# Kernel optimization log

Measured on AMD Instinct MI355X. Metric: run time of the kernel, lower is better.

Reference implementation:

```python
import jax, jax.numpy as jnp
import numpy as np

B, S, D_X, D_H = 1024, 512, 128, 128
A_VOCAB, A_EMB, T_VOCAB, T_EMB = 100, 32, 4, 16
GRU_IN = D_X + A_EMB + T_EMB + 1  # 177
Y_IN = D_H + D_X + A_EMB + T_EMB  # 304


def _lin_init(key, d_in, d_out):
    k1, k2 = jax.random.split(key)
    lim = 1.0 / np.sqrt(d_in)
    W = jax.random.uniform(k1, (d_out, d_in), minval=-lim, maxval=lim, dtype=jnp.float32)
    b = jax.random.uniform(k2, (d_out,), minval=-lim, maxval=lim, dtype=jnp.float32)
    return W, b


def setup_inputs() -> dict:
    key = jax.random.key(0)
    ks = jax.random.split(key, 16)
    x = jax.random.normal(ks[0], (B, D_X), dtype=jnp.float32)
    a = jax.random.randint(ks[1], (B, S), 0, A_VOCAB)
    t = jax.random.randint(ks[2], (B, S), 0, T_VOCAB)
    y = jax.random.uniform(ks[3], (B, S), dtype=jnp.float32)
    mask = jnp.ones((B, S), dtype=jnp.float32)

    xW, xb = _lin_init(ks[4], D_X, D_X)                 # x_proj
    a_emb = jax.random.normal(ks[5], (A_VOCAB, A_EMB), dtype=jnp.float32)
    t_emb = jax.random.normal(ks[6], (T_VOCAB, T_EMB), dtype=jnp.float32)
    W_ih, b_ih = _lin_init(ks[7], GRU_IN, 3 * D_H)      # GRUCell input weights
    W_hh, b_hh = _lin_init(ks[8], D_H, 3 * D_H)         # GRUCell hidden weights
    h0W, h0b = _lin_init(ks[9], D_X, D_H)               # h0 MLP
    tW1, tb1 = _lin_init(ks[10], D_H, D_H)              # t_head
    tW2, tb2 = _lin_init(ks[11], D_H, T_VOCAB)
    yW1, yb1 = _lin_init(ks[12], Y_IN, D_H)             # y_head
    yW2, yb2 = _lin_init(ks[13], D_H, 1)
    return {
        'x': x, 'a': a, 't': t, 'y': y, 'mask': mask,
        'xW': xW, 'xb': xb, 'a_emb': a_emb, 't_emb': t_emb,
        'W_ih': W_ih, 'b_ih': b_ih, 'W_hh': W_hh, 'b_hh': b_hh,
        'h0W': h0W, 'h0b': h0b,
        'tW1': tW1, 'tb1': tb1, 'tW2': tW2, 'tb2': tb2,
        'yW1': yW1, 'yb1': yb1, 'yW2': yW2, 'yb2': yb2,
    }


def _crn_forward(x, y, mask, xW, xb, a_emb, t_emb, W_ih, b_ih, W_hh, b_hh,
                 h0W, h0b, tW1, tb1, tW2, tb2, yW1, yb1, yW2, yb2, a, t):
    gelu = lambda v: jax.nn.gelu(v, approximate=False)
    x_enc = x @ xW.T + xb                       # [B, D_X]
    h = jnp.tanh(x_enc @ h0W.T + h0b)           # [B, D_H]
    a_e = a_emb[a]                              # [B, S, A_EMB]
    t_e = t_emb[t]                              # [B, S, T_EMB]
    y3 = y[..., None]                           # [B, S, 1]

    # time-major slices for scan
    a_e_t = jnp.swapaxes(a_e, 0, 1)
    t_e_t = jnp.swapaxes(t_e, 0, 1)
    y_t = jnp.swapaxes(y3, 0, 1)
    m_t = jnp.swapaxes(mask, 0, 1)[..., None]   # [S, B, 1]

    def step(h, inp):
        ae, te, yt, m = inp
        # grad_reverse is identity in forward; dropout off (eval)
        t_logits = gelu(h @ tW1.T + tb1) @ tW2.T + tb2          # [B, T_VOCAB]
        y_in = jnp.concatenate([h, x_enc, ae, te], axis=-1)
        y_logits = gelu(y_in @ yW1.T + yb1) @ yW2.T + yb2        # [B, 1]
        upd = jnp.concatenate([x_enc, ae, te, yt], axis=-1)      # [B, GRU_IN]
        gx = upd @ W_ih.T + b_ih
        gh = h @ W_hh.T + b_hh
        r = jax.nn.sigmoid(gx[:, :D_H] + gh[:, :D_H])
        z = jax.nn.sigmoid(gx[:, D_H:2 * D_H] + gh[:, D_H:2 * D_H])
        n = jnp.tanh(gx[:, 2 * D_H:] + r * gh[:, 2 * D_H:])
        h_next = (1.0 - z) * n + z * h
        h_new = m * h_next + (1.0 - m) * h
        return h_new, (y_logits, t_logits, h)

    _, (y_seq, t_seq, h_seq) = jax.lax.scan(step, h, (a_e_t, t_e_t, y_t, m_t))
    # back to batch-major [B, S, ...]
    return (jnp.swapaxes(y_seq, 0, 1), jnp.swapaxes(t_seq, 0, 1), jnp.swapaxes(h_seq, 0, 1))


def reference(x, a, t, y, mask, xW, xb, a_emb, t_emb, W_ih, b_ih, W_hh, b_hh,
              h0W, h0b, tW1, tb1, tW2, tb2, yW1, yb1, yW2, yb2):
    return _crn_forward(x, y, mask, xW, xb, a_emb, t_emb, W_ih, b_ih, W_hh, b_hh,
                        h0W, h0b, tW1, tb1, tW2, tb2, yW1, yb1, yW2, yb2, a, t)
```

## Files before the change

### kernel.cpp

```cpp
#include <hip/hip_runtime.h>
#include <math.h>

#define SLEN 512

typedef _Float16 half8 __attribute__((ext_vector_type(8)));
typedef _Float16 half2v __attribute__((ext_vector_type(2)));
typedef __fp16 fp16x2 __attribute__((ext_vector_type(2)));
typedef float f32x4 __attribute__((ext_vector_type(4)));
typedef unsigned int uint;

union U4H8 { uint4 u; half8 h; };
union UH2 { uint u; half2v v; fp16x2 p; };

static __device__ __forceinline__ uint packh2(float a, float b){
  UH2 x; x.p = __builtin_amdgcn_cvt_pkrtz(a, b); return x.u;
}
static __device__ __forceinline__ float loh(uint u){ UH2 x; x.u=u; return (float)x.v[0]; }
static __device__ __forceinline__ float hih(uint u){ UH2 x; x.u=u; return (float)x.v[1]; }
static __device__ __forceinline__ half8 ld_h8(const uint* p){
  U4H8 x; x.u = *(const uint4*)p; return x.h;
}
static __device__ __forceinline__ float rcpf(float x){ return __builtin_amdgcn_rcpf(x); }
static __device__ __forceinline__ float sigm(float v){ return rcpf(1.0f+__expf(-v)); }
static __device__ __forceinline__ float tanh_f(float v){ return 1.0f - 2.0f*rcpf(__expf(2.0f*v)+1.0f); }
static __device__ __forceinline__ float gelu_exact(float v){
  return 0.5f*v*(1.0f+erff(v*0.7071067811865475f));
}
#define MFMA(a,b,c) __builtin_amdgcn_mfma_f32_16x16x32_f16((a),(b),(c),0,0,0)

__global__ void k_sample(const float* __restrict__ x, const float* __restrict__ xW, const float* __restrict__ xb,
                         const float* __restrict__ h0W, const float* __restrict__ h0b,
                         const float* __restrict__ W_ih, const float* __restrict__ b_ih, const float* __restrict__ b_hh,
                         const float* __restrict__ yW1, const float* __restrict__ yb1,
                         float* __restrict__ w_h0, float* __restrict__ w_xgx, float* __restrict__ w_yx)
{
  const int b = blockIdx.x, tid = threadIdx.x;
  __shared__ float sx[128];
  __shared__ float sxe[128];
  if (tid < 128) sx[tid] = x[b*128+tid];
  __syncthreads();
  if (tid < 128) {
    float acc = xb[tid];
    #pragma unroll 8
    for (int j=0;j<128;++j) acc += xW[tid*128+j]*sx[j];
    sxe[tid] = acc;
  }
  __syncthreads();
  {
    const int o = tid;
    float acc = b_ih[o] + (o < 256 ? b_hh[o] : 0.f);
    #pragma unroll 8
    for (int j=0;j<128;++j) acc += W_ih[o*177+j]*sxe[j];
    w_xgx[b*384+o] = acc;
  }
  if (tid < 128) {
    float acc = h0b[tid];
    #pragma unroll 8
    for (int j=0;j<128;++j) acc += h0W[tid*128+j]*sxe[j];
    w_h0[b*128+tid] = tanhf(acc);
    float a2 = yb1[tid];
    #pragma unroll 8
    for (int j=0;j<128;++j) a2 += yW1[tid*304+128+j]*sxe[j];
    w_yx[b*128+tid] = a2;
  }
}

__global__ __launch_bounds__(384,1) void k_recur(
  const float* __restrict__ W_hh, const float* __restrict__ W_ih, const float* __restrict__ b_hh,
  const int* __restrict__ a, const int* __restrict__ tt,
  const float* __restrict__ yy, const float* __restrict__ mask,
  const float* __restrict__ w_h0, const float* __restrict__ w_xgx,
  const float* __restrict__ a_emb, const float* __restrict__ t_emb,
  float* __restrict__ o_h, uint* __restrict__ h16)
{
  const int tid = threadIdx.x;
  const int wv = tid>>6, lane = tid&63, q = lane>>4, c = lane&15;
  const int g = wv>>1, H = wv&1;
  const int b0 = blockIdx.x*16;
  const int rowbase = g*128 + H*64;

  __shared__ __align__(16) uint s_h[2][16*68];
  __shared__ __align__(16) uint s_ext[2][16*36];
  __shared__ __align__(16) uint s_rz[2][1024];
  __shared__ __align__(16) uint s_chunk[2][1024];
  __shared__ __align__(16) uint s_al[1600];
  __shared__ __align__(16) uint s_te[32];

  half8 wf[24];
  #pragma unroll
  for (int t4=0;t4<4;++t4) {
    const int row = rowbase + t4*16 + c;
    #pragma unroll
    for (int kt=0;kt<4;++kt) {
      const float4* wp = (const float4*)(W_hh + row*128 + kt*32 + q*8);
      float4 v0 = wp[0], v1 = wp[1];
      half8 hv;
      hv[0]=(_Float16)v0.x; hv[1]=(_Float16)v0.y; hv[2]=(_Float16)v0.z; hv[3]=(_Float16)v0.w;
      hv[4]=(_Float16)v1.x; hv[5]=(_Float16)v1.y; hv[6]=(_Float16)v1.z; hv[7]=(_Float16)v1.w;
      wf[t4*6+kt] = hv;
    }
    #pragma unroll
    for (int kt=4;kt<6;++kt) {
      half8 hv;
      #pragma unroll
      for (int j=0;j<8;++j) {
        int k2 = (kt-4)*32 + q*8 + j;
        float v = (k2 < 49) ? W_ih[row*177 + 128 + k2] : 0.f;
        hv[j] = (_Float16)v;
      }
      wf[t4*6+kt] = hv;
    }
  }
  f32x4 xg[4];
  #pragma unroll
  for (int t4=0;t4<4;++t4)
    #pragma unroll
    for (int r=0;r<4;++r)
      xg[t4][r] = w_xgx[(b0+c)*384 + rowbase + t4*16 + q*4 + r];
  f32x4 bhh[4]; float hm[16];
  if (g==2) {
    #pragma unroll
    for (int t4=0;t4<4;++t4)
      #pragma unroll
      for (int r=0;r<4;++r) {
        bhh[t4][r] = b_hh[256 + H*64 + t4*16 + q*4 + r];
        hm[t4*4+r] = w_h0[(b0+c)*128 + H*64 + t4*16 + q*4 + r];
      }
  }
  for (int d = tid; d < 1600; d += 384) {
    int row = d>>4, col = d&15;
    s_al[d] = packh2(a_emb[row*32+2*col], a_emb[row*32+2*col+1]);
  }
  if (tid < 32) {
    int row = tid>>3, col = tid&7;
    s_te[tid] = packh2(t_emb[row*16+2*col], t_emb[row*16+2*col+1]);
  }
  uint4 cr0, cr1, cr2, cr3;
  if (wv==0) {
    const uint* bp = (q==0) ? (const uint*)a : (q==1) ? (const uint*)tt
                   : (q==2) ? (const uint*)yy : (const uint*)mask;
    const uint4* p = (const uint4*)(bp + (size_t)(b0+c)*512);
    cr0=p[0]; cr1=p[1]; cr2=p[2]; cr3=p[3];
    uint4* dst = (uint4*)&s_chunk[0][q*256 + c*16];
    dst[0]=cr0; dst[1]=cr1; dst[2]=cr2; dst[3]=cr3;
  }
  if (g==2) {
    #pragma unroll
    for (int t4=0;t4<4;++t4) {
      int base = c*68 + H*32 + t4*8 + q*2;
      s_h[0][base]   = packh2(hm[t4*4+0], hm[t4*4+1]);
      s_h[0][base+1] = packh2(hm[t4*4+2], hm[t4*4+3]);
    }
  }
  __syncthreads();
  if (g==0) {
    int av = (int)s_chunk[0][c*16];
    int tv = (int)s_chunk[0][256 + c*16];
    uint yu = s_chunk[0][512 + c*16];
    float yv = __uint_as_float(yu);
    #pragma unroll
    for (int i=0;i<4;++i) {
      int d = H*16 + q*4 + i;
      uint u;
      if (d < 16) u = s_al[av*16 + d];
      else if (d < 24) u = s_te[tv*8 + (d-16)];
      else if (d == 24) u = packh2(yv, 0.f);
      else u = 0u;
      s_ext[0][c*36 + d] = u;
    }
  }
  __syncthreads();

  f32x4 acc[4], acc2[4];

  for (int s=0; s<SLEN; ++s) {
    const int pb = s&1;
    half8 hb[4], eb[2];
    #pragma unroll
    for (int kt=0;kt<4;++kt) hb[kt] = ld_h8(&s_h[pb][c*68 + kt*16 + q*4]);
    #pragma unroll
    for (int e=0;e<2;++e)    eb[e]  = ld_h8(&s_ext[pb][c*36 + e*16 + q*4]);

    if (g < 2) {
      if (g==1 && s>0) {
        const int ob = (s-1)&1;
        const int smp = H*8 + (lane>>3), ch = lane&7;
        const uint* hp = &s_h[ob][smp*68 + ch*8];
        const size_t pr = (size_t)(b0+smp)*SLEN + (s-1);
        if (h16) {
          uint4* hq = (uint4*)(h16 + pr*64 + ch*8);
          hq[0] = *(const uint4*)(hp);
          hq[1] = *(const uint4*)(hp + 4);
        } else {
          float* op = o_h + pr*128 + ch*16;
          #pragma unroll
          for (int i2=0;i2<2;++i2) {
            uint4 u = *(const uint4*)(hp + i2*4);
            float4 f0 = make_float4(loh(u.x), hih(u.x), loh(u.y), hih(u.y));
            float4 f1 = make_float4(loh(u.z), hih(u.z), loh(u.w), hih(u.w));
            *(float4*)(op + i2*8)     = f0;
            *(float4*)(op + i2*8 + 4) = f1;
          }
        }
      }
      #pragma unroll
      for (int t4=0;t4<4;++t4) acc[t4] = xg[t4];
      #pragma unroll
      for (int kt=0;kt<6;++kt) {
        half8 bsel = (kt<4) ? hb[kt] : eb[kt-4];
        #pragma unroll
        for (int t4=0;t4<4;++t4) acc[t4] = MFMA(wf[t4*6+kt], bsel, acc[t4]);
      }
      #pragma unroll
      for (int t4=0;t4<4;++t4)
        #pragma unroll
        for (int pr=0;pr<2;++pr) {
          float s0 = sigm(acc[t4][2*pr]), s1 = sigm(acc[t4][2*pr+1]);
          s_rz[g][(((H*4+t4)*2+pr)*4+q)*16 + c] = packh2(s0, s1);
        }
      if (wv==0) {
        if ((s&15)==8 && s<490) {
          const int s0n = ((s>>4)+1)*16;
          const uint* bp = (q==0) ? (const uint*)a : (q==1) ? (const uint*)tt
                         : (q==2) ? (const uint*)yy : (const uint*)mask;
          const uint4* p = (const uint4*)(bp + (size_t)(b0+c)*512 + s0n);
          cr0=p[0]; cr1=p[1]; cr2=p[2]; cr3=p[3];
        }
        if ((s&15)==9 && s<491) {
          uint4* dst = (uint4*)&s_chunk[((s>>4)+1)&1][q*256 + c*16];
          dst[0]=cr0; dst[1]=cr1; dst[2]=cr2; dst[3]=cr3;
        }
      }
    } else {
      #pragma unroll
      for (int t4=0;t4<4;++t4) { acc[t4] = bhh[t4]; acc2[t4] = xg[t4]; }
      #pragma unroll
      for (int kt=0;kt<4;++kt)
        #pragma unroll
        for (int t4=0;t4<4;++t4) acc[t4] = MFMA(wf[t4*6+kt], hb[kt], acc[t4]);
      #pragma unroll
      for (int kt=4;kt<6;++kt)
        #pragma unroll
        for (int t4=0;t4<4;++t4) acc2[t4] = MFMA(wf[t4*6+kt], eb[kt-4], acc2[t4]);
    }
    __syncthreads();
    if (g==2) {
      const float mval = __uint_as_float(s_chunk[(s>>4)&1][768 + c*16 + (s&15)]);
      #pragma unroll
      for (int t4=0;t4<4;++t4)
        #pragma unroll
        for (int pr=0;pr<2;++pr) {
          const int slot = (((H*4+t4)*2+pr)*4+q)*16 + c;
          uint ru = s_rz[0][slot], zu = s_rz[1][slot];
          const int i0 = t4*4 + 2*pr;
          float n0 = tanh_f(acc2[t4][2*pr]   + loh(ru)*acc[t4][2*pr]);
          float n1 = tanh_f(acc2[t4][2*pr+1] + hih(ru)*acc[t4][2*pr+1]);
          float h0o = hm[i0], h1o = hm[i0+1];
          float hn0 = n0 + loh(zu)*(h0o - n0);
          float hn1 = n1 + hih(zu)*(h1o - n1);
          hm[i0]   = h0o + mval*(hn0 - h0o);
          hm[i0+1] = h1o + mval*(hn1 - h1o);
        }
      const int nb = (s+1)&1;
      #pragma unroll
      for (int t4=0;t4<4;++t4) {
        int base = c*68 + H*32 + t4*8 + q*2;
        s_h[nb][base]   = packh2(hm[t4*4+0], hm[t4*4+1]);
        s_h[nb][base+1] = packh2(hm[t4*4+2], hm[t4*4+3]);
      }
    } else if (g==0 && s < SLEN-1) {
      const int sn = s+1;
      const int par2 = (sn>>4)&1, st = sn&15;
      int av = (int)s_chunk[par2][c*16 + st];
      int tv = (int)s_chunk[par2][256 + c*16 + st];
      float yv = __uint_as_float(s_chunk[par2][512 + c*16 + st]);
      #pragma unroll
      for (int i=0;i<4;++i) {
        int d = H*16 + q*4 + i;
        uint u;
        if (d < 16) u = s_al[av*16 + d];
        else if (d < 24) u = s_te[tv*8 + (d-16)];
        else if (d == 24) u = packh2(yv, 0.f);
        else u = 0u;
        s_ext[(s+1)&1][c*36 + d] = u;
      }
    }
    __syncthreads();
  }
  if (g==1) {
    const int ob = (SLEN-1)&1;
    const int smp = H*8 + (lane>>3), ch = lane&7;
    const uint* hp = &s_h[ob][smp*68 + ch*8];
    const size_t pr = (size_t)(b0+smp)*SLEN + (SLEN-1);
    if (h16) {
      uint4* hq = (uint4*)(h16 + pr*64 + ch*8);
      hq[0] = *(const uint4*)(hp);
      hq[1] = *(const uint4*)(hp + 4);
    } else {
      float* op = o_h + pr*128 + ch*16;
      #pragma unroll
      for (int i2=0;i2<2;++i2) {
        uint4 u = *(const uint4*)(hp + i2*4);
        float4 f0 = make_float4(loh(u.x), hih(u.x), loh(u.y), hih(u.y));
        float4 f1 = make_float4(loh(u.z), hih(u.z), loh(u.w), hih(u.w));
        *(float4*)(op + i2*8)     = f0;
        *(float4*)(op + i2*8 + 4) = f1;
      }
    }
  }
}

template<bool H16>
__global__ __launch_bounds__(256,1) void k_heads(
  const float* __restrict__ tW1, const float* __restrict__ tb1,
  const float* __restrict__ tW2, const float* __restrict__ tb2,
  const float* __restrict__ yW1, const float* __restrict__ yW2, const float* __restrict__ yb2,
  const int* __restrict__ a, const int* __restrict__ tt,
  const float* __restrict__ w_yx,
  const float* __restrict__ a_emb, const float* __restrict__ t_emb,
  const float* __restrict__ h_f32, const uint* __restrict__ h16,
  float* __restrict__ o_y, float* __restrict__ o_t, float* __restrict__ o_h)
{
  const int tid = threadIdx.x;
  const int wv = tid>>6, lane = tid&63, q = lane>>4, c = lane&15;
  const bool isY = (wv >= 2);
  const int p0 = blockIdx.x*1024;
  const int b0 = blockIdx.x*2;

  __shared__ __align__(16) uint s_al[100*20];
  __shared__ __align__(16) uint s_te[32];
  __shared__ __align__(16) uint s_gb[4][16*68];

  for (int d = tid; d < 1600; d += 256) {
    int row = d>>4, col = d&15;
    s_al[row*20+col] = packh2(a_emb[row*32+2*col], a_emb[row*32+2*col+1]);
  }
  if (tid < 32) {
    int row = tid>>3, col = tid&7;
    s_te[row*8+col] = packh2(t_emb[row*16+2*col], t_emb[row*16+2*col+1]);
  }

  half8 wf[48];
  const float* W1 = isY ? yW1 : tW1;
  const int w1stride = isY ? 304 : 128;
  #pragma unroll
  for (int ut=0;ut<8;++ut) {
    const int unit = ut*16 + c;
    #pragma unroll
    for (int kt=0;kt<4;++kt) {
      const float4* wp = (const float4*)(W1 + unit*w1stride + kt*32 + q*8);
      float4 v0 = wp[0], v1 = wp[1];
      half8 hv;
      hv[0]=(_Float16)v0.x; hv[1]=(_Float16)v0.y; hv[2]=(_Float16)v0.z; hv[3]=(_Float16)v0.w;
      hv[4]=(_Float16)v1.x; hv[5]=(_Float16)v1.y; hv[6]=(_Float16)v1.z; hv[7]=(_Float16)v1.w;
      wf[ut*6+kt] = hv;
    }
    #pragma unroll
    for (int kt=4;kt<6;++kt) {
      half8 hv;
      #pragma unroll
      for (int j=0;j<8;++j) {
        int k2 = (kt-4)*32 + q*8 + j;
        float v = (isY && k2 < 48) ? yW1[unit*304 + 256 + k2] : 0.f;
        hv[j] = (_Float16)v;
      }
      wf[ut*6+kt] = hv;
    }
  }
  half8 w2f[4];
  #pragma unroll
  for (int kt=0;kt<4;++kt) {
    half8 hv;
    #pragma unroll
    for (int j=0;j<8;++j) {
      float v = 0.f;
      if (!isY && c < 4) v = tW2[c*128 + kt*32 + q*8 + j];
      if ( isY && c == 0) v = yW2[kt*32 + q*8 + j];
      hv[j] = (_Float16)v;
    }
    w2f[kt] = hv;
  }
  float tb2r[4]; float yb2s = yb2[0];
  #pragma unroll
  for (int r=0;r<4;++r) tb2r[r] = tb2[r];

  __syncthreads();

  #pragma unroll 1
  for (int bh=0; bh<2; ++bh) {
    f32x4 bsr[8];
    #pragma unroll
    for (int ut=0;ut<8;++ut)
      #pragma unroll
      for (int r=0;r<4;++r)
        bsr[ut][r] = isY ? w_yx[(b0+bh)*128 + ut*16 + q*4 + r]
                         : tb1[ut*16 + q*4 + r];

    #pragma unroll 1
    for (int ti=0; ti<16; ++ti) {
      const int tile = bh*32 + ti*2 + (wv&1);
      const int p = p0 + tile*16 + c;

      half8 hb[4], eb[2];
      if (H16) {
        const uint* hp = h16 + (size_t)p*64;
        #pragma unroll
        for (int kt=0;kt<4;++kt) hb[kt] = ld_h8(hp + kt*16 + q*4);
      } else {
        const float* hp = h_f32 + (size_t)p*128;
        #pragma unroll
        for (int kt=0;kt<4;++kt) {
          const float4* fp = (const float4*)(hp + kt*32 + q*8);
          float4 v0 = fp[0], v1 = fp[1];
          half8 hv;
          hv[0]=(_Float16)v0.x; hv[1]=(_Float16)v0.y; hv[2]=(_Float16)v0.z; hv[3]=(_Float16)v0.w;
          hv[4]=(_Float16)v1.x; hv[5]=(_Float16)v1.y; hv[6]=(_Float16)v1.z; hv[7]=(_Float16)v1.w;
          hb[kt] = hv;
        }
      }
      if (H16 && !isY) {
        float* op = o_h + (size_t)p*128;
        #pragma unroll
        for (int kt=0;kt<4;++kt) {
          float4 f0 = make_float4((float)hb[kt][0], (float)hb[kt][1], (float)hb[kt][2], (float)hb[kt][3]);
          float4 f1 = make_float4((float)hb[kt][4], (float)hb[kt][5], (float)hb[kt][6], (float)hb[kt][7]);
          *(float4*)(op + kt*32 + q*8)     = f0;
          *(float4*)(op + kt*32 + q*8 + 4) = f1;
        }
      }
      if (isY) {
        const int av = a[p], tv = tt[p];
        eb[0] = ld_h8(&s_al[av*20 + q*4]);
        if (q < 2) eb[1] = ld_h8(&s_te[tv*8 + q*4]);
        else {
          half8 z;
          #pragma unroll
          for (int j=0;j<8;++j) z[j] = (_Float16)0.f;
          eb[1] = z;
        }
      }

      f32x4 acc[8];
      #pragma unroll
      for (int ut=0;ut<8;++ut) acc[ut] = bsr[ut];
      #pragma unroll
      for (int kt=0;kt<4;++kt)
        #pragma unroll
        for (int ut=0;ut<8;++ut) acc[ut] = MFMA(wf[ut*6+kt], hb[kt], acc[ut]);
      if (isY) {
        #pragma unroll
        for (int kt=4;kt<6;++kt)
          #pragma unroll
          for (int ut=0;ut<8;++ut) acc[ut] = MFMA(wf[ut*6+kt], eb[kt-4], acc[ut]);
      }

      #pragma unroll
      for (int ut=0;ut<8;++ut)
        #pragma unroll
        for (int pr=0;pr<2;++pr) {
          float g0 = gelu_exact(acc[ut][2*pr]);
          float g1 = gelu_exact(acc[ut][2*pr+1]);
          s_gb[wv][c*68 + 8*ut + 2*q + pr] = packh2(g0, g1);
        }
      f32x4 a2; a2[0]=0.f; a2[1]=0.f; a2[2]=0.f; a2[3]=0.f;
      #pragma unroll
      for (int kt=0;kt<4;++kt) {
        half8 gb = ld_h8(&s_gb[wv][c*68 + kt*16 + q*4]);
        a2 = MFMA(w2f[kt], gb, a2);
      }
      if (lane < 16) {
        if (!isY) {
          float4 o = make_float4(a2[0]+tb2r[0], a2[1]+tb2r[1], a2[2]+tb2r[2], a2[3]+tb2r[3]);
          *(float4*)&o_t[(size_t)p*4] = o;
        } else {
          o_y[p] = a2[0] + yb2s;
        }
      }
    }
  }
}

extern "C" void kernel_launch(void* const* d_in, const int* in_sizes, int n_in,
                              void* d_out, int out_size, void* d_ws, size_t ws_size,
                              hipStream_t stream) {
  (void)in_sizes; (void)n_in; (void)out_size;
  const float* x     = (const float*)d_in[0];
  const int*   a     = (const int*)  d_in[1];
  const int*   tt    = (const int*)  d_in[2];
  const float* y     = (const float*)d_in[3];
  const float* mask  = (const float*)d_in[4];
  const float* xW    = (const float*)d_in[5];
  const float* xb    = (const float*)d_in[6];
  const float* a_emb = (const float*)d_in[7];
  const float* t_emb = (const float*)d_in[8];
  const float* W_ih  = (const float*)d_in[9];
  const float* b_ih  = (const float*)d_in[10];
  const float* W_hh  = (const float*)d_in[11];
  const float* b_hh  = (const float*)d_in[12];
  const float* h0W   = (const float*)d_in[13];
  const float* h0b   = (const float*)d_in[14];
  const float* tW1   = (const float*)d_in[15];
  const float* tb1   = (const float*)d_in[16];
  const float* tW2   = (const float*)d_in[17];
  const float* tb2   = (const float*)d_in[18];
  const float* yW1   = (const float*)d_in[19];
  const float* yb1   = (const float*)d_in[20];
  const float* yW2   = (const float*)d_in[21];
  const float* yb2   = (const float*)d_in[22];

  float* o_y = (float*)d_out;
  float* o_t = o_y + 524288;
  float* o_h = o_y + 2621440;

  float* ws    = (float*)d_ws;
  float* w_h0  = ws;
  float* w_xgx = ws + 131072;
  float* w_yx  = ws + 524288;

  const size_t H16_BYTES = (size_t)524288 * 256;
  uint* h16 = nullptr;
  if (ws_size >= (size_t)655360*4 + H16_BYTES) h16 = (uint*)(ws + 655360);

  k_sample<<<1024, 384, 0, stream>>>(x, xW, xb, h0W, h0b, W_ih, b_ih, b_hh, yW1, yb1,
                                     w_h0, w_xgx, w_yx);
  k_recur<<<64, 384, 0, stream>>>(W_hh, W_ih, b_hh, a, tt, y, mask,
                                  w_h0, w_xgx, a_emb, t_emb, o_h, h16);
  if (h16)
    k_heads<true><<<512, 256, 0, stream>>>(tW1, tb1, tW2, tb2, yW1, yW2, yb2, a, tt,
                                           w_yx, a_emb, t_emb, o_h, h16, o_y, o_t, o_h);
  else
    k_heads<false><<<512, 256, 0, stream>>>(tW1, tb1, tW2, tb2, yW1, yW2, yb2, a, tt,
                                            w_yx, a_emb, t_emb, o_h, nullptr, o_y, o_t, o_h);
}
```

Baseline: 1.225 ms.

## Split head hidden units across wave pairs and replace syncthreads with raw barriers

Measured after the change: 1.354 ms. 10.5% more time.

```diff
diff --git a/kernel.cpp b/kernel.cpp
--- a/kernel.cpp
+++ b/kernel.cpp
@@ -27,6 +27,13 @@
   return 0.5f*v*(1.0f+erff(v*0.7071067811865475f));
 }
 #define MFMA(a,b,c) __builtin_amdgcn_mfma_f32_16x16x32_f16((a),(b),(c),0,0,0)
+
+static __device__ __forceinline__ void wg_barrier(){
+  __builtin_amdgcn_sched_barrier(0);
+  asm volatile("s_waitcnt lgkmcnt(0)" ::: "memory");
+  __builtin_amdgcn_s_barrier();
+  __builtin_amdgcn_sched_barrier(0);
+}
 
 __global__ void k_sample(const float* __restrict__ x, const float* __restrict__ xW, const float* __restrict__ xb,
                          const float* __restrict__ h0W, const float* __restrict__ h0b,
@@ -243,7 +250,7 @@
         #pragma unroll
         for (int t4=0;t4<4;++t4) acc2[t4] = MFMA(wf[t4*6+kt], eb[kt-4], acc2[t4]);
     }
-    __syncthreads();
+    wg_barrier();
     if (g==2) {
       const float mval = __uint_as_float(s_chunk[(s>>4)&1][768 + c*16 + (s&15)]);
       #pragma unroll
@@ -285,7 +292,7 @@
         s_ext[(s+1)&1][c*36 + d] = u;
       }
     }
-    __syncthreads();
+    wg_barrier();
   }
   if (g==1) {
     const int ob = (SLEN-1)&1;
@@ -311,7 +318,7 @@
 }
 
 template<bool H16>
-__global__ __launch_bounds__(256,1) void k_heads(
+__global__ __launch_bounds__(256,2) void k_heads(
   const float* __restrict__ tW1, const float* __restrict__ tb1,
   const float* __restrict__ tW2, const float* __restrict__ tb2,
   const float* __restrict__ yW1, const float* __restrict__ yW2, const float* __restrict__ yb2,
@@ -324,12 +331,14 @@
   const int tid = threadIdx.x;
   const int wv = tid>>6, lane = tid&63, q = lane>>4, c = lane&15;
   const bool isY = (wv >= 2);
+  const int uh = wv&1;
+  const int pair = wv>>1;
   const int p0 = blockIdx.x*1024;
   const int b0 = blockIdx.x*2;
 
   __shared__ __align__(16) uint s_al[100*20];
   __shared__ __align__(16) uint s_te[32];
-  __shared__ __align__(16) uint s_gb[4][16*68];
+  __shared__ __align__(16) uint s_gb[2][2][16*68];
 
   for (int d = tid; d < 1600; d += 256) {
     int row = d>>4, col = d&15;
@@ -340,12 +349,12 @@
     s_te[row*8+col] = packh2(t_emb[row*16+2*col], t_emb[row*16+2*col+1]);
   }
 
-  half8 wf[48];
+  half8 wf[24];
   const float* W1 = isY ? yW1 : tW1;
   const int w1stride = isY ? 304 : 128;
   #pragma unroll
-  for (int ut=0;ut<8;++ut) {
-    const int unit = ut*16 + c;
+  for (int ut=0;ut<4;++ut) {
+    const int unit = uh*64 + ut*16 + c;
     #pragma unroll
     for (int kt=0;kt<4;++kt) {
       const float4* wp = (const float4*)(W1 + unit*w1stride + kt*32 + q*8);
@@ -388,20 +397,21 @@
 
   #pragma unroll 1
   for (int bh=0; bh<2; ++bh) {
-    f32x4 bsr[8];
-    #pragma unroll
-    for (int ut=0;ut<8;++ut)
+    f32x4 bsr[4];
+    #pragma unroll
+    for (int ut=0;ut<4;++ut)
       #pragma unroll
       for (int r=0;r<4;++r)
-        bsr[ut][r] = isY ? w_yx[(b0+bh)*128 + ut*16 + q*4 + r]
-                         : tb1[ut*16 + q*4 + r];
+        bsr[ut][r] = isY ? w_yx[(b0+bh)*128 + uh*64 + ut*16 + q*4 + r]
+                         : tb1[uh*64 + ut*16 + q*4 + r];
 
     #pragma unroll 1
-    for (int ti=0; ti<16; ++ti) {
-      const int tile = bh*32 + ti*2 + (wv&1);
+    for (int ti=0; ti<32; ++ti) {
+      const int tile = bh*32 + ti;
+      const int par = ti&1;
       const int p = p0 + tile*16 + c;
 
-      half8 hb[4], eb[2];
+      half8 hb[4];
       if (H16) {
         const uint* hp = h16 + (size_t)p*64;
         #pragma unroll
@@ -421,14 +431,24 @@
       if (H16 && !isY) {
         float* op = o_h + (size_t)p*128;
         #pragma unroll
-        for (int kt=0;kt<4;++kt) {
+        for (int kk=0;kk<2;++kk) {
+          const int kt = uh*2 + kk;
           float4 f0 = make_float4((float)hb[kt][0], (float)hb[kt][1], (float)hb[kt][2], (float)hb[kt][3]);
           float4 f1 = make_float4((float)hb[kt][4], (float)hb[kt][5], (float)hb[kt][6], (float)hb[kt][7]);
           *(float4*)(op + kt*32 + q*8)     = f0;
           *(float4*)(op + kt*32 + q*8 + 4) = f1;
         }
       }
+
+      f32x4 acc[4];
+      #pragma unroll
+      for (int ut=0;ut<4;++ut) acc[ut] = bsr[ut];
+      #pragma unroll
+      for (int kt=0;kt<4;++kt)
+        #pragma unroll
+        for (int ut=0;ut<4;++ut) acc[ut] = MFMA(wf[ut*6+kt], hb[kt], acc[ut]);
       if (isY) {
+        half8 eb[2];
         const int av = a[p], tv = tt[p];
         eb[0] = ld_h8(&s_al[av*20 + q*4]);
         if (q < 2) eb[1] = ld_h8(&s_te[tv*8 + q*4]);
@@ -438,37 +458,29 @@
           for (int j=0;j<8;++j) z[j] = (_Float16)0.f;
           eb[1] = z;
         }
-      }
-
-      f32x4 acc[8];
-      #pragma unroll
-      for (int ut=0;ut<8;++ut) acc[ut] = bsr[ut];
-      #pragma unroll
-      for (int kt=0;kt<4;++kt)
-        #pragma unroll
-        for (int ut=0;ut<8;++ut) acc[ut] = MFMA(wf[ut*6+kt], hb[kt], acc[ut]);
-      if (isY) {
         #pragma unroll
         for (int kt=4;kt<6;++kt)
           #pragma unroll
-          for (int ut=0;ut<8;++ut) acc[ut] = MFMA(wf[ut*6+kt], eb[kt-4], acc[ut]);
-      }
-
-      #pragma unroll
-      for (int ut=0;ut<8;++ut)
+          for (int ut=0;ut<4;++ut) acc[ut] = MFMA(wf[ut*6+kt], eb[kt-4], acc[ut]);
+      }
+
+      #pragma unroll
+      for (int ut=0;ut<4;++ut)
         #pragma unroll
         for (int pr=0;pr<2;++pr) {
           float g0 = gelu_exact(acc[ut][2*pr]);
           float g1 = gelu_exact(acc[ut][2*pr+1]);
-          s_gb[wv][c*68 + 8*ut + 2*q + pr] = packh2(g0, g1);
-        }
+          s_gb[pair][par][c*68 + uh*32 + ut*8 + 2*q + pr] = packh2(g0, g1);
+        }
+      wg_barrier();
+
       f32x4 a2; a2[0]=0.f; a2[1]=0.f; a2[2]=0.f; a2[3]=0.f;
       #pragma unroll
       for (int kt=0;kt<4;++kt) {
-        half8 gb = ld_h8(&s_gb[wv][c*68 + kt*16 + q*4]);
+        half8 gb = ld_h8(&s_gb[pair][par][c*68 + kt*16 + q*4]);
         a2 = MFMA(w2f[kt], gb, a2);
       }
-      if (lane < 16) {
+      if (uh==0 && lane < 16) {
         if (!isY) {
           float4 o = make_float4(a2[0]+tb2r[0], a2[1]+tb2r[1], a2[2]+tb2r[2], a2[3]+tb2r[3]);
           *(float4*)&o_t[(size_t)p*4] = o;
```
